# Kernel optimization log

Measured on AMD Instinct MI355X. Metric: run time of the kernel, lower is better.

Reference implementation:

```python
import jax, jax.numpy as jnp
import numpy as np

SEQ_LEN, BATCH, DIM = 128, 128, 1024

def setup_inputs() -> dict:
    key = jax.random.key(0)
    k1, k2, k3, k4 = jax.random.split(key, 4)
    scale = 1.0 / np.sqrt(DIM)
    return {
        "x": jax.random.normal(k1, (SEQ_LEN, BATCH, DIM), dtype=jnp.float32),
        "h0": jax.random.normal(k2, (BATCH, DIM), dtype=jnp.float32),
        "Wx": jax.random.normal(k3, (DIM, DIM), dtype=jnp.float32) * scale,
        "Wh": jax.random.normal(k4, (DIM, DIM), dtype=jnp.float32) * scale,
        "b": jnp.zeros((DIM,), dtype=jnp.float32),
    }

def reference(x, h0, Wx, Wh, b):
    # Vanilla tanh RNN cell scanned over seq_len (dropout is identity at keep_prob=1).
    # Precompute the input projection for all timesteps in one big GEMM.
    xp = jnp.einsum('sbi,ij->sbj', x, Wx) + b  # [S, B, H]
    def step(h, xp_t):
        h_new = jnp.tanh(xp_t + h @ Wh)
        return h_new, h_new
    _, hs = jax.lax.scan(step, h0, xp)
    return hs  # [seq_len, batch, hidden]: stacked hidden states
```

## Files before the change

### kernel.cpp

```cpp
#include <hip/hip_runtime.h>
#include <math.h>


#define DIM 1024
#define BATCH 128
#define SEQ 128
#define BD (BATCH * DIM)
#define NBLK 128
#define HSTR 1032
#define FLAGSTR 16
#define XNB 256
#define HXGRP 16384

typedef __attribute__((ext_vector_type(8))) short bf16x8;
typedef __attribute__((ext_vector_type(4))) float f32x4;

static __device__ __forceinline__ unsigned short f2bf_rne(float f) {
    unsigned u = __builtin_bit_cast(unsigned, f);
    unsigned r = (u + 0x7FFFu + ((u >> 16) & 1u)) >> 16;
    return (unsigned short)r;
}
static __device__ __forceinline__ float bf2f(unsigned short h) {
    return __builtin_bit_cast(float, ((unsigned)h) << 16);
}

static __device__ __forceinline__ void split_pair(
    unsigned long long v, unsigned& hp, unsigned& lp)
{
    const unsigned u0 = (unsigned)v;
    const unsigned u1 = (unsigned)(v >> 32);
    const float f0 = __builtin_bit_cast(float, u0);
    const float f1 = __builtin_bit_cast(float, u1);
    hp = (u0 >> 16) | (u1 & 0xFFFF0000u);
    const float r0 = f0 - __builtin_bit_cast(float, u0 & 0xFFFF0000u);
    const float r1 = f1 - __builtin_bit_cast(float, u1 & 0xFFFF0000u);
    lp = (unsigned)f2bf_rne(r0) | ((unsigned)f2bf_rne(r1) << 16);
}

__global__ __launch_bounds__(512) void xp_pers(
    const float* __restrict__ x,
    const float* __restrict__ Wx,
    const float* __restrict__ bias,
    float* __restrict__ out)
{
    __shared__ unsigned short hHi[16 * HSTR];
    __shared__ unsigned short hLo[16 * HSTR];
    __shared__ f32x4 redS[256];

    const int tid = threadIdx.x;
    const int bid = blockIdx.x;
    const int g   = bid & 15;
    const int ct  = bid >> 4;
    const int tg  = g >> 3;
    const int bt  = g & 7;
    const int B0  = bt * 16;
    const int Cb  = ct * 64;
    const int NT  = SEQ / 2;

    const int w = tid >> 6;
    const int l = tid & 63;
    const int n = l & 15;
    const int q = l >> 4;
    const int cb = Cb + (w >> 1) * 16;
    const int K0 = (w & 1) * 512;

    bf16x8 Bhi[16], Blo[16];
    #pragma unroll
    for (int s = 0; s < 16; ++s) {
        bf16x8 hi, lo;
        #pragma unroll
        for (int j = 0; j < 8; ++j) {
            const int k = K0 + 32 * s + q * 8 + j;
            const float wv = Wx[(size_t)k * DIM + cb + n];
            const unsigned short h16 = f2bf_rne(wv);
            hi[j] = (short)h16;
            lo[j] = (short)f2bf_rne(wv - bf2f(h16));
        }
        Bhi[s] = hi;
        Blo[s] = lo;
    }
    const float bv = bias[cb + n];

    const int sr = tid >> 5;
    const int su = tid & 31;

    {
        const float* xT = x + (size_t)(tg * NT) * BD + (size_t)B0 * DIM;
        const unsigned long long* srow =
            (const unsigned long long*)(xT + (size_t)sr * DIM);
        unsigned short* dh = &hHi[sr * HSTR];
        unsigned short* dl = &hLo[sr * HSTR];
        #pragma unroll
        for (int i = 0; i < 16; ++i) {
            unsigned hp, lp;
            split_pair(srow[su + 32 * i], hp, lp);
            *(unsigned*)(dh + 2 * (su + 32 * i)) = hp;
            *(unsigned*)(dl + 2 * (su + 32 * i)) = lp;
        }
    }

    for (int tt = 0; tt < NT; ++tt) {
        const int t = tg * NT + tt;
        float* outT = out + (size_t)t * BD;

        unsigned long long xr[16];
        if (tt + 1 < NT) {
            const float* xN = x + (size_t)(t + 1) * BD + (size_t)B0 * DIM;
            const unsigned long long* srow =
                (const unsigned long long*)(xN + (size_t)sr * DIM);
            #pragma unroll
            for (int i = 0; i < 16; ++i) xr[i] = srow[su + 32 * i];
        }

        __syncthreads();

        f32x4 acc = {0.f, 0.f, 0.f, 0.f};
        {
            const unsigned short* rh = &hHi[(l & 15) * HSTR + K0];
            const unsigned short* rl = &hLo[(l & 15) * HSTR + K0];
            #pragma unroll
            for (int s = 0; s < 16; ++s) {
                const bf16x8 ah = *(const bf16x8*)(rh + 32 * s + 8 * q);
                const bf16x8 al = *(const bf16x8*)(rl + 32 * s + 8 * q);
                acc = __builtin_amdgcn_mfma_f32_16x16x32_bf16(ah, Bhi[s], acc, 0, 0, 0);
                acc = __builtin_amdgcn_mfma_f32_16x16x32_bf16(al, Bhi[s], acc, 0, 0, 0);
                acc = __builtin_amdgcn_mfma_f32_16x16x32_bf16(ah, Blo[s], acc, 0, 0, 0);
            }
        }

        if (w & 1) redS[(w >> 1) * 64 + l] = acc;
        __syncthreads();

        if (!(w & 1)) {
            const f32x4 p = redS[(w >> 1) * 64 + l];
            #pragma unroll
            for (int i = 0; i < 4; ++i)
                outT[(size_t)(B0 + q * 4 + i) * DIM + cb + n] = acc[i] + p[i] + bv;
        }

        if (tt + 1 < NT) {
            unsigned short* dh = &hHi[sr * HSTR];
            unsigned short* dl = &hLo[sr * HSTR];
            #pragma unroll
            for (int i = 0; i < 16; ++i) {
                unsigned hp, lp;
                split_pair(xr[i], hp, lp);
                *(unsigned*)(dh + 2 * (su + 32 * i)) = hp;
                *(unsigned*)(dl + 2 * (su + 32 * i)) = lp;
            }
        }
    }
}

__global__ __launch_bounds__(512) void rnn_scan(
    const float* __restrict__ h0,
    const float* __restrict__ Wh,
    float* out,
    unsigned* tags,
    unsigned short* hX)
{
    __shared__ unsigned short hS[16 * HSTR];
    __shared__ f32x4 redS[256];

    const int tid = threadIdx.x;
    const int p   = blockIdx.x;
    const int bt  = p & 7;
    const int ct  = p >> 3;
    const int B0  = bt * 16;
    const int Cb  = ct * 64;

    const int w = tid >> 6;
    const int l = tid & 63;
    const int n = l & 15;
    const int q = l >> 4;
    const int cb = Cb + (w >> 1) * 16;
    const int K0 = (w & 1) * 512;

    bf16x8 Bhi[16], Blo[16];
    #pragma unroll
    for (int s = 0; s < 16; ++s) {
        bf16x8 hi, lo;
        #pragma unroll
        for (int j = 0; j < 8; ++j) {
            const int k = K0 + 32 * s + q * 8 + j;
            const float wv = Wh[(size_t)k * DIM + cb + n];
            const unsigned short h16 = f2bf_rne(wv);
            hi[j] = (short)h16;
            lo[j] = (short)f2bf_rne(wv - bf2f(h16));
        }
        Bhi[s] = hi;
        Blo[s] = lo;
    }

    const int sr = tid >> 5;
    const int su = tid & 31;
    const int qq = tid & 3;
    const int c0 = (tid >> 2) & 127;

    const int myslot = bt * 64 + ct * 4 + (w >> 1);
    const unsigned* tg0 = &tags[(bt * 64 + (c0 >> 2)) * FLAGSTR];
    const unsigned* tg1 = &tags[(bt * 64 + 32 + (c0 >> 2)) * FLAGSTR];

    for (int t = 0; t < SEQ; ++t) {
        float* outT = out + (size_t)t * BD;

        float xpv[4];
        if (!(w & 1)) {
            #pragma unroll
            for (int i = 0; i < 4; ++i)
                xpv[i] = __builtin_nontemporal_load(
                    &outT[(size_t)(B0 + q * 4 + i) * DIM + cb + n]);
        }

        if (t == 0) {
            const float* hsrc = h0 + (size_t)B0 * DIM;
            const unsigned long long* srow =
                (const unsigned long long*)(hsrc + (size_t)sr * DIM);
            unsigned short* drow = &hS[sr * HSTR];
            #pragma unroll
            for (int i = 0; i < 16; ++i) {
                const unsigned long long v = srow[su + 32 * i];
                const float f0 = __builtin_bit_cast(float, (unsigned)(v & 0xFFFFFFFFull));
                const float f1 = __builtin_bit_cast(float, (unsigned)(v >> 32));
                const unsigned pk =
                    (unsigned)f2bf_rne(f0) | ((unsigned)f2bf_rne(f1) << 16);
                *(unsigned*)(drow + 2 * (su + 32 * i)) = pk;
            }
        } else {
            const unsigned need = (unsigned)t;
            while (__hip_atomic_load(tg0, __ATOMIC_RELAXED,
                                     __HIP_MEMORY_SCOPE_AGENT) < need)
                __builtin_amdgcn_s_sleep(1);
            while (__hip_atomic_load(tg1, __ATOMIC_RELAXED,
                                     __HIP_MEMORY_SCOPE_AGENT) < need)
                __builtin_amdgcn_s_sleep(1);
            asm volatile("" ::: "memory");

            const unsigned short* gX = hX + (size_t)((t - 1) & 1) * (8 * HXGRP)
                                          + (size_t)bt * HXGRP;
            #pragma unroll
            for (int half = 0; half < 2; ++half) {
                const int cp = c0 + half * 128;
                unsigned long long L[4];
                #pragma unroll
                for (int cc = 0; cc < 4; ++cc)
                    L[cc] = __hip_atomic_load(
                        (const unsigned long long*)(gX + (size_t)(4 * cp + cc) * 16 + qq * 4),
                        __ATOMIC_RELAXED, __HIP_MEMORY_SCOPE_AGENT);
                #pragma unroll
                for (int i = 0; i < 2; ++i) {
                    const unsigned a0 = (unsigned)(L[0] >> (32 * i));
                    const unsigned a1 = (unsigned)(L[1] >> (32 * i));
                    const unsigned a2 = (unsigned)(L[2] >> (32 * i));
                    const unsigned a3 = (unsigned)(L[3] >> (32 * i));
                    const unsigned r0w0 = (a0 & 0xFFFFu) | (a1 << 16);
                    const unsigned r0w1 = (a2 & 0xFFFFu) | (a3 << 16);
                    const unsigned r1w0 = (a0 >> 16) | (a1 & 0xFFFF0000u);
                    const unsigned r1w1 = (a2 >> 16) | (a3 & 0xFFFF0000u);
                    *(unsigned long long*)&hS[(4 * qq + 2 * i) * HSTR + 4 * cp] =
                        (unsigned long long)r0w0 | ((unsigned long long)r0w1 << 32);
                    *(unsigned long long*)&hS[(4 * qq + 2 * i + 1) * HSTR + 4 * cp] =
                        (unsigned long long)r1w0 | ((unsigned long long)r1w1 << 32);
                }
            }
        }

        __syncthreads();

        f32x4 acc = {0.f, 0.f, 0.f, 0.f};
        {
            const unsigned short* hrow = &hS[(l & 15) * HSTR + K0];
            #pragma unroll
            for (int s = 0; s < 16; ++s) {
                const bf16x8 a = *(const bf16x8*)(hrow + 32 * s + 8 * q);
                acc = __builtin_amdgcn_mfma_f32_16x16x32_bf16(a, Bhi[s], acc, 0, 0, 0);
                acc = __builtin_amdgcn_mfma_f32_16x16x32_bf16(a, Blo[s], acc, 0, 0, 0);
            }
        }

        if (w & 1) redS[(w >> 1) * 64 + l] = acc;
        __syncthreads();

        if (!(w & 1)) {
            const f32x4 pp = redS[(w >> 1) * 64 + l];
            const float v0 = tanhf(acc[0] + pp[0] + xpv[0]);
            const float v1 = tanhf(acc[1] + pp[1] + xpv[1]);
            const float v2 = tanhf(acc[2] + pp[2] + xpv[2]);
            const float v3 = tanhf(acc[3] + pp[3] + xpv[3]);

            if (t < SEQ - 1) {
                const unsigned p0 = (unsigned)f2bf_rne(v0) | ((unsigned)f2bf_rne(v1) << 16);
                const unsigned p1 = (unsigned)f2bf_rne(v2) | ((unsigned)f2bf_rne(v3) << 16);
                unsigned short* gW = hX + (size_t)(t & 1) * (8 * HXGRP)
                                        + (size_t)bt * HXGRP;
                __hip_atomic_store(
                    (unsigned long long*)(gW + (size_t)(cb + n) * 16 + q * 4),
                    (unsigned long long)p0 | ((unsigned long long)p1 << 32),
                    __ATOMIC_RELAXED, __HIP_MEMORY_SCOPE_AGENT);
                asm volatile("s_waitcnt vmcnt(0)" ::: "memory");
                if (l == 0)
                    __hip_atomic_store(&tags[myslot * FLAGSTR], (unsigned)(t + 1),
                                       __ATOMIC_RELAXED, __HIP_MEMORY_SCOPE_AGENT);
            }

            __builtin_nontemporal_store(v0, &outT[(size_t)(B0 + q * 4 + 0) * DIM + cb + n]);
            __builtin_nontemporal_store(v1, &outT[(size_t)(B0 + q * 4 + 1) * DIM + cb + n]);
            __builtin_nontemporal_store(v2, &outT[(size_t)(B0 + q * 4 + 2) * DIM + cb + n]);
            __builtin_nontemporal_store(v3, &outT[(size_t)(B0 + q * 4 + 3) * DIM + cb + n]);
        }
    }
}

extern "C" void kernel_launch(void* const* d_in, const int* in_sizes, int n_in,
                              void* d_out, int out_size, void* d_ws, size_t ws_size,
                              hipStream_t stream) {
    const float* x  = (const float*)d_in[0];
    const float* h0 = (const float*)d_in[1];
    const float* Wx = (const float*)d_in[2];
    const float* Wh = (const float*)d_in[3];
    const float* b  = (const float*)d_in[4];
    float* out = (float*)d_out;
    unsigned* tags = (unsigned*)d_ws;
    unsigned short* hX = (unsigned short*)((char*)d_ws + 32768);

    hipMemsetAsync(d_ws, 0, 512 * FLAGSTR * sizeof(unsigned), stream);

    xp_pers<<<dim3(XNB), dim3(512), 0, stream>>>(x, Wx, b, out);

    rnn_scan<<<dim3(NBLK), dim3(512), 0, stream>>>(h0, Wh, out, tags, hX);
}
```

Baseline: 772.3 us.

## Drop K-split in recurrent step: 4 waves own full K, double-buffer hidden state

The recurrent kernel changes from 8 waves splitting K in two with an LDS reduction to 4 waves that each hold the full 1024-deep Wh slice in registers (64 bf16x8 fragments). This removes the second __syncthreads and the redS reduction per timestep. The LDS hidden-state buffer is double-buffered by timestep parity, and two accumulators interleave the MFMA chains. The trade-off is a much higher register load per thread, with spill risk, and each thread now does twice the MFMA and gather work with half the threads.

```diff
diff --git a/kernel.cpp b/kernel.cpp
--- a/kernel.cpp
+++ b/kernel.cpp
@@ -152,15 +152,14 @@
     }
 }
 
-__global__ __launch_bounds__(512) void rnn_scan(
+__global__ __launch_bounds__(256, 1) void rnn_scan(
     const float* __restrict__ h0,
     const float* __restrict__ Wh,
     float* out,
     unsigned* tags,
     unsigned short* hX)
 {
-    __shared__ unsigned short hS[16 * HSTR];
-    __shared__ f32x4 redS[256];
+    __shared__ unsigned short hS[2][16 * HSTR];
 
     const int tid = threadIdx.x;
     const int p   = blockIdx.x;
@@ -173,16 +172,15 @@
     const int l = tid & 63;
     const int n = l & 15;
     const int q = l >> 4;
-    const int cb = Cb + (w >> 1) * 16;
-    const int K0 = (w & 1) * 512;
-
-    bf16x8 Bhi[16], Blo[16];
+    const int cb = Cb + w * 16;
+
+    bf16x8 Bhi[32], Blo[32];
     #pragma unroll
-    for (int s = 0; s < 16; ++s) {
+    for (int s = 0; s < 32; ++s) {
         bf16x8 hi, lo;
         #pragma unroll
         for (int j = 0; j < 8; ++j) {
-            const int k = K0 + 32 * s + q * 8 + j;
+            const int k = 32 * s + q * 8 + j;
             const float wv = Wh[(size_t)k * DIM + cb + n];
             const unsigned short h16 = f2bf_rne(wv);
             hi[j] = (short)h16;
@@ -192,122 +190,112 @@
         Blo[s] = lo;
     }
 
-    const int sr = tid >> 5;
-    const int su = tid & 31;
-    const int qq = tid & 3;
-    const int c0 = (tid >> 2) & 127;
-
-    const int myslot = bt * 64 + ct * 4 + (w >> 1);
-    const unsigned* tg0 = &tags[(bt * 64 + (c0 >> 2)) * FLAGSTR];
-    const unsigned* tg1 = &tags[(bt * 64 + 32 + (c0 >> 2)) * FLAGSTR];
+    const int cu = tid;
+    const unsigned* tgp = &tags[(bt * 64 + (cu >> 2)) * FLAGSTR];
+    const int myslot = bt * 64 + ct * 4 + w;
+
+    const int sr = tid >> 4;
+    const int su = tid & 15;
 
     for (int t = 0; t < SEQ; ++t) {
         float* outT = out + (size_t)t * BD;
 
         float xpv[4];
-        if (!(w & 1)) {
-            #pragma unroll
-            for (int i = 0; i < 4; ++i)
-                xpv[i] = __builtin_nontemporal_load(
-                    &outT[(size_t)(B0 + q * 4 + i) * DIM + cb + n]);
-        }
+        #pragma unroll
+        for (int i = 0; i < 4; ++i)
+            xpv[i] = __builtin_nontemporal_load(
+                &outT[(size_t)(B0 + q * 4 + i) * DIM + cb + n]);
 
         if (t == 0) {
             const float* hsrc = h0 + (size_t)B0 * DIM;
             const unsigned long long* srow =
                 (const unsigned long long*)(hsrc + (size_t)sr * DIM);
-            unsigned short* drow = &hS[sr * HSTR];
-            #pragma unroll
-            for (int i = 0; i < 16; ++i) {
-                const unsigned long long v = srow[su + 32 * i];
+            unsigned short* drow = &hS[0][sr * HSTR];
+            #pragma unroll
+            for (int i = 0; i < 32; ++i) {
+                const unsigned long long v = srow[su + 16 * i];
                 const float f0 = __builtin_bit_cast(float, (unsigned)(v & 0xFFFFFFFFull));
                 const float f1 = __builtin_bit_cast(float, (unsigned)(v >> 32));
                 const unsigned pk =
                     (unsigned)f2bf_rne(f0) | ((unsigned)f2bf_rne(f1) << 16);
-                *(unsigned*)(drow + 2 * (su + 32 * i)) = pk;
+                *(unsigned*)(drow + 2 * (su + 16 * i)) = pk;
             }
         } else {
             const unsigned need = (unsigned)t;
-            while (__hip_atomic_load(tg0, __ATOMIC_RELAXED,
-                                     __HIP_MEMORY_SCOPE_AGENT) < need)
-                __builtin_amdgcn_s_sleep(1);
-            while (__hip_atomic_load(tg1, __ATOMIC_RELAXED,
+            while (__hip_atomic_load(tgp, __ATOMIC_RELAXED,
                                      __HIP_MEMORY_SCOPE_AGENT) < need)
                 __builtin_amdgcn_s_sleep(1);
             asm volatile("" ::: "memory");
 
             const unsigned short* gX = hX + (size_t)((t - 1) & 1) * (8 * HXGRP)
                                           + (size_t)bt * HXGRP;
-            #pragma unroll
-            for (int half = 0; half < 2; ++half) {
-                const int cp = c0 + half * 128;
-                unsigned long long L[4];
+            unsigned long long L[4][4];
+            #pragma unroll
+            for (int c = 0; c < 4; ++c)
                 #pragma unroll
-                for (int cc = 0; cc < 4; ++cc)
-                    L[cc] = __hip_atomic_load(
-                        (const unsigned long long*)(gX + (size_t)(4 * cp + cc) * 16 + qq * 4),
+                for (int qd = 0; qd < 4; ++qd)
+                    L[c][qd] = __hip_atomic_load(
+                        (const unsigned long long*)(gX + (size_t)(4 * cu + c) * 16 + qd * 4),
                         __ATOMIC_RELAXED, __HIP_MEMORY_SCOPE_AGENT);
+
+            unsigned short* dst = &hS[t & 1][0];
+            #pragma unroll
+            for (int qd = 0; qd < 4; ++qd) {
                 #pragma unroll
-                for (int i = 0; i < 2; ++i) {
-                    const unsigned a0 = (unsigned)(L[0] >> (32 * i));
-                    const unsigned a1 = (unsigned)(L[1] >> (32 * i));
-                    const unsigned a2 = (unsigned)(L[2] >> (32 * i));
-                    const unsigned a3 = (unsigned)(L[3] >> (32 * i));
-                    const unsigned r0w0 = (a0 & 0xFFFFu) | (a1 << 16);
-                    const unsigned r0w1 = (a2 & 0xFFFFu) | (a3 << 16);
-                    const unsigned r1w0 = (a0 >> 16) | (a1 & 0xFFFF0000u);
-                    const unsigned r1w1 = (a2 >> 16) | (a3 & 0xFFFF0000u);
-                    *(unsigned long long*)&hS[(4 * qq + 2 * i) * HSTR + 4 * cp] =
-                        (unsigned long long)r0w0 | ((unsigned long long)r0w1 << 32);
-                    *(unsigned long long*)&hS[(4 * qq + 2 * i + 1) * HSTR + 4 * cp] =
-                        (unsigned long long)r1w0 | ((unsigned long long)r1w1 << 32);
+                for (int rr = 0; rr < 4; ++rr) {
+                    const int r = 4 * qd + rr;
+                    const int sh = 16 * rr;
+                    const unsigned long long row =
+                          ((L[0][qd] >> sh) & 0xFFFFull)
+                        | (((L[1][qd] >> sh) & 0xFFFFull) << 16)
+                        | (((L[2][qd] >> sh) & 0xFFFFull) << 32)
+                        | (((L[3][qd] >> sh) & 0xFFFFull) << 48);
+                    *(unsigned long long*)&dst[r * HSTR + 4 * cu] = row;
                 }
             }
         }
 
         __syncthreads();
 
-        f32x4 acc = {0.f, 0.f, 0.f, 0.f};
+        f32x4 a0 = {0.f, 0.f, 0.f, 0.f};
+        f32x4 a1 = {0.f, 0.f, 0.f, 0.f};
         {
-            const unsigned short* hrow = &hS[(l & 15) * HSTR + K0];
-            #pragma unroll
-            for (int s = 0; s < 16; ++s) {
-                const bf16x8 a = *(const bf16x8*)(hrow + 32 * s + 8 * q);
-                acc = __builtin_amdgcn_mfma_f32_16x16x32_bf16(a, Bhi[s], acc, 0, 0, 0);
-                acc = __builtin_amdgcn_mfma_f32_16x16x32_bf16(a, Blo[s], acc, 0, 0, 0);
-            }
-        }
-
-        if (w & 1) redS[(w >> 1) * 64 + l] = acc;
-        __syncthreads();
-
-        if (!(w & 1)) {
-            const f32x4 pp = redS[(w >> 1) * 64 + l];
-            const float v0 = tanhf(acc[0] + pp[0] + xpv[0]);
-            const float v1 = tanhf(acc[1] + pp[1] + xpv[1]);
-            const float v2 = tanhf(acc[2] + pp[2] + xpv[2]);
-            const float v3 = tanhf(acc[3] + pp[3] + xpv[3]);
-
-            if (t < SEQ - 1) {
-                const unsigned p0 = (unsigned)f2bf_rne(v0) | ((unsigned)f2bf_rne(v1) << 16);
-                const unsigned p1 = (unsigned)f2bf_rne(v2) | ((unsigned)f2bf_rne(v3) << 16);
-                unsigned short* gW = hX + (size_t)(t & 1) * (8 * HXGRP)
-                                        + (size_t)bt * HXGRP;
-                __hip_atomic_store(
-                    (unsigned long long*)(gW + (size_t)(cb + n) * 16 + q * 4),
-                    (unsigned long long)p0 | ((unsigned long long)p1 << 32),
-                    __ATOMIC_RELAXED, __HIP_MEMORY_SCOPE_AGENT);
-                asm volatile("s_waitcnt vmcnt(0)" ::: "memory");
-                if (l == 0)
-                    __hip_atomic_store(&tags[myslot * FLAGSTR], (unsigned)(t + 1),
-                                       __ATOMIC_RELAXED, __HIP_MEMORY_SCOPE_AGENT);
-            }
-
-            __builtin_nontemporal_store(v0, &outT[(size_t)(B0 + q * 4 + 0) * DIM + cb + n]);
-            __builtin_nontemporal_store(v1, &outT[(size_t)(B0 + q * 4 + 1) * DIM + cb + n]);
-            __builtin_nontemporal_store(v2, &outT[(size_t)(B0 + q * 4 + 2) * DIM + cb + n]);
-            __builtin_nontemporal_store(v3, &outT[(size_t)(B0 + q * 4 + 3) * DIM + cb + n]);
-        }
+            const unsigned short* hrow = &hS[t & 1][(l & 15) * HSTR];
+            #pragma unroll
+            for (int s = 0; s < 32; s += 2) {
+                const bf16x8 x0 = *(const bf16x8*)(hrow + 32 * s + 8 * q);
+                const bf16x8 x1 = *(const bf16x8*)(hrow + 32 * (s + 1) + 8 * q);
+                a0 = __builtin_amdgcn_mfma_f32_16x16x32_bf16(x0, Bhi[s], a0, 0, 0, 0);
+                a1 = __builtin_amdgcn_mfma_f32_16x16x32_bf16(x1, Bhi[s + 1], a1, 0, 0, 0);
+                a0 = __builtin_amdgcn_mfma_f32_16x16x32_bf16(x0, Blo[s], a0, 0, 0, 0);
+                a1 = __builtin_amdgcn_mfma_f32_16x16x32_bf16(x1, Blo[s + 1], a1, 0, 0, 0);
+            }
+        }
+
+        const float v0 = tanhf(a0[0] + a1[0] + xpv[0]);
+        const float v1 = tanhf(a0[1] + a1[1] + xpv[1]);
+        const float v2 = tanhf(a0[2] + a1[2] + xpv[2]);
+        const float v3 = tanhf(a0[3] + a1[3] + xpv[3]);
+
+        if (t < SEQ - 1) {
+            const unsigned p0 = (unsigned)f2bf_rne(v0) | ((unsigned)f2bf_rne(v1) << 16);
+            const unsigned p1 = (unsigned)f2bf_rne(v2) | ((unsigned)f2bf_rne(v3) << 16);
+            unsigned short* gW = hX + (size_t)(t & 1) * (8 * HXGRP)
+                                    + (size_t)bt * HXGRP;
+            __hip_atomic_store(
+                (unsigned long long*)(gW + (size_t)(cb + n) * 16 + q * 4),
+                (unsigned long long)p0 | ((unsigned long long)p1 << 32),
+                __ATOMIC_RELAXED, __HIP_MEMORY_SCOPE_AGENT);
+            asm volatile("s_waitcnt vmcnt(0)" ::: "memory");
+            if (l == 0)
+                __hip_atomic_store(&tags[myslot * FLAGSTR], (unsigned)(t + 1),
+                                   __ATOMIC_RELAXED, __HIP_MEMORY_SCOPE_AGENT);
+        }
+
+        __builtin_nontemporal_store(v0, &outT[(size_t)(B0 + q * 4 + 0) * DIM + cb + n]);
+        __builtin_nontemporal_store(v1, &outT[(size_t)(B0 + q * 4 + 1) * DIM + cb + n]);
+        __builtin_nontemporal_store(v2, &outT[(size_t)(B0 + q * 4 + 2) * DIM + cb + n]);
+        __builtin_nontemporal_store(v3, &outT[(size_t)(B0 + q * 4 + 3) * DIM + cb + n]);
     }
 }
 
@@ -327,5 +315,5 @@
 
     xp_pers<<<dim3(XNB), dim3(512), 0, stream>>>(x, Wx, b, out);
 
-    rnn_scan<<<dim3(NBLK), dim3(512), 0, stream>>>(h0, Wh, out, tags, hX);
-}
+    rnn_scan<<<dim3(NBLK), dim3(256), 0, stream>>>(h0, Wh, out, tags, hX);
+}
```

Result: slower. 1.019 ms (+32.0%).
